# Kernel tuning notes

Hardware: AMD Instinct MI355X
Metric: run time of the kernel (lower is better)

The kernel has to match this reference:

```python
import jax, jax.numpy as jnp
import numpy as np

NUM_POINTS = 2048
FEAT_DIMS = 512
BATCH = 32


def setup_inputs() -> dict:
    key = jax.random.key(0)
    ks = jax.random.split(key, 7)
    glf = jax.random.normal(ks[0], (BATCH, FEAT_DIMS, 1), dtype=jnp.float32)
    # Per-position linear weights (one Conv1d(k=1) per position, fused):
    # W[p, out, in], b[p, out]. Scale like PyTorch Conv1d default init.
    W1 = jax.random.normal(ks[1], (NUM_POINTS, 32, FEAT_DIMS), dtype=jnp.float32) * (1.0 / np.sqrt(FEAT_DIMS))
    b1 = jax.random.normal(ks[2], (NUM_POINTS, 32), dtype=jnp.float32) * 0.01
    W2 = jax.random.normal(ks[3], (NUM_POINTS, 8, 32), dtype=jnp.float32) * (1.0 / np.sqrt(32))
    b2 = jax.random.normal(ks[4], (NUM_POINTS, 8), dtype=jnp.float32) * 0.01
    W3 = jax.random.normal(ks[5], (NUM_POINTS, 3, 8), dtype=jnp.float32) * (1.0 / np.sqrt(8))
    b3 = jax.random.normal(ks[6], (NUM_POINTS, 3), dtype=jnp.float32) * 0.01
    return {"glf": glf, "W1": W1, "b1": b1, "W2": W2, "b2": b2, "W3": W3, "b3": b3}


def _fc_layer(x, W, b):
    # x: [B, Cin, P], W: [P, Cout, Cin], b: [P, Cout] -> [B, Cout, P]
    return jnp.einsum('bip,poi->bop', x, W) + b.T[None, :, :]


def reference(glf, W1, b1, W2, b2, W3, b3):
    # glf: [B, feat_dims, 1] -> repeat along positions
    x = jnp.broadcast_to(glf, (glf.shape[0], glf.shape[1], NUM_POINTS))
    x = _fc_layer(x, W1, b1)  # [B, 32, P]
    x = _fc_layer(x, W2, b2)  # [B, 8, P]
    x = _fc_layer(x, W3, b3)  # [B, 3, P]  (seg_class == 0)
    return x
```

## Files before the change

kernel.cpp:

```cpp
#include <hip/hip_runtime.h>

#define NUM_POINTS 2048
#define FEAT 512
#define BATCH 32
#define POS_PER_BLOCK 2

using v8s = __attribute__((ext_vector_type(8))) short;
using v4f = __attribute__((ext_vector_type(4))) float;

static __device__ __forceinline__ short f2bf(float x) {
  unsigned u = __float_as_uint(x);
  u += 0x7FFFu + ((u >> 16) & 1u);
  return (short)(u >> 16);
}

static __device__ __forceinline__ v8s cvt8(const float* p) {
  float4 f0 = *(const float4*)(p);
  float4 f1 = *(const float4*)(p + 4);
  v8s r;
  r[0] = f2bf(f0.x); r[1] = f2bf(f0.y); r[2] = f2bf(f0.z); r[3] = f2bf(f0.w);
  r[4] = f2bf(f1.x); r[5] = f2bf(f1.y); r[6] = f2bf(f1.z); r[7] = f2bf(f1.w);
  return r;
}

__global__ void build_bfrag(const float* __restrict__ glf, short* __restrict__ frag) {
  int i = blockIdx.x * 256 + threadIdx.x;
  int j = i & 7;
  int l = (i >> 3) & 63;
  int nt = (i >> 9) & 1;
  int ks = i >> 10;
  int b = nt * 16 + (l & 15);
  int k = ks * 32 + ((l >> 4) << 3) + j;
  frag[i] = f2bf(glf[b * FEAT + k]);
}

__global__ void __launch_bounds__(256) fcdec_main(
    const float* __restrict__ W1, const float* __restrict__ b1,
    const float* __restrict__ W2, const float* __restrict__ b2,
    const float* __restrict__ W3, const float* __restrict__ b3,
    const short* __restrict__ bfrag, float* __restrict__ out) {
  __shared__ float h1s[POS_PER_BLOCK][32][33];

  const int t = threadIdx.x;
  const int w = t >> 6;
  const int l = t & 63;
  const int lp = w >> 1;
  const int mt = w & 1;
  const int p = blockIdx.x * POS_PER_BLOCK + lp;
  const int lrow = l & 15;
  const int lk = (l >> 4) << 3;

  v4f acc[2] = {};
  const float* A0 = W1 + ((size_t)p * 32u + mt * 16 + lrow) * FEAT + lk;

  #pragma unroll 4
  for (int ks = 0; ks < 16; ++ks) {
    v8s a = cvt8(A0 + ks * 32);
    v8s bv0 = *(const v8s*)(bfrag + (((ks * 2 + 0) * 64 + l) << 3));
    v8s bv1 = *(const v8s*)(bfrag + (((ks * 2 + 1) * 64 + l) << 3));
    acc[0] = __builtin_amdgcn_mfma_f32_16x16x32_bf16(a, bv0, acc[0], 0, 0, 0);
    acc[1] = __builtin_amdgcn_mfma_f32_16x16x32_bf16(a, bv1, acc[1], 0, 0, 0);
  }

  #pragma unroll
  for (int nt = 0; nt < 2; ++nt)
    #pragma unroll
    for (int r = 0; r < 4; ++r) {
      int o = mt * 16 + ((l >> 4) << 2) + r;
      int b = nt * 16 + (l & 15);
      h1s[lp][o][b] = acc[nt][r] + b1[p * 32 + o];
    }
  __syncthreads();

  if (t < POS_PER_BLOCK * BATCH) {
    const int tp = t >> 5;
    const int b = t & 31;
    const int pg = blockIdx.x * POS_PER_BLOCK + tp;
    float h2[8];
    #pragma unroll
    for (int o8 = 0; o8 < 8; ++o8) {
      float s = b2[pg * 8 + o8];
      const float* w2 = W2 + (size_t)(pg * 8 + o8) * 32;
      #pragma unroll
      for (int i = 0; i < 32; ++i) s += w2[i] * h1s[tp][i][b];
      h2[o8] = s;
    }
    #pragma unroll
    for (int c = 0; c < 3; ++c) {
      float s = b3[pg * 3 + c];
      const float* w3 = W3 + (size_t)(pg * 3 + c) * 8;
      #pragma unroll
      for (int j = 0; j < 8; ++j) s += w3[j] * h2[j];
      out[(size_t)(b * 3 + c) * NUM_POINTS + pg] = s;
    }
  }
}

extern "C" void kernel_launch(void* const* d_in, const int* in_sizes, int n_in,
                              void* d_out, int out_size, void* d_ws, size_t ws_size,
                              hipStream_t stream) {
  const float* glf = (const float*)d_in[0];
  const float* W1  = (const float*)d_in[1];
  const float* b1  = (const float*)d_in[2];
  const float* W2  = (const float*)d_in[3];
  const float* b2  = (const float*)d_in[4];
  const float* W3  = (const float*)d_in[5];
  const float* b3  = (const float*)d_in[6];
  float* out = (float*)d_out;
  short* frag = (short*)d_ws;

  hipLaunchKernelGGL(build_bfrag, dim3(64), dim3(256), 0, stream, glf, frag);
  hipLaunchKernelGGL(fcdec_main, dim3(NUM_POINTS / POS_PER_BLOCK), dim3(256), 0, stream,
                     W1, b1, W2, b2, W3, b3, frag, out);
}
```

Before: 34.31 us.

## Stage W1 tiles into LDS via direct global-to-LDS loads, one position per block

Each block now handles a single position. It bulk-loads that position's 32x512 W1 slice into a 64KB LDS tile using global_load_lds with an XOR swizzle, then each wave reads swizzled float4s from LDS and runs one 16x16 MFMA tile. Layer 2 is spread across all 256 threads, with an extra LDS stage and barrier before layer 3. The aim is wide, coalesced streaming of the dominant W1 traffic. The cost is 64KB of LDS per block, which caps occupancy, plus no overlap between the load phase and the compute phase within a block.

```diff
diff --git a/kernel.cpp b/kernel.cpp
--- a/kernel.cpp
+++ b/kernel.cpp
@@ -3,24 +3,17 @@
 #define NUM_POINTS 2048
 #define FEAT 512
 #define BATCH 32
-#define POS_PER_BLOCK 2
 
 using v8s = __attribute__((ext_vector_type(8))) short;
 using v4f = __attribute__((ext_vector_type(4))) float;
+
+typedef __attribute__((address_space(3))) float lds_f;
+typedef const __attribute__((address_space(1))) float gbl_f;
 
 static __device__ __forceinline__ short f2bf(float x) {
   unsigned u = __float_as_uint(x);
   u += 0x7FFFu + ((u >> 16) & 1u);
   return (short)(u >> 16);
-}
-
-static __device__ __forceinline__ v8s cvt8(const float* p) {
-  float4 f0 = *(const float4*)(p);
-  float4 f1 = *(const float4*)(p + 4);
-  v8s r;
-  r[0] = f2bf(f0.x); r[1] = f2bf(f0.y); r[2] = f2bf(f0.z); r[3] = f2bf(f0.w);
-  r[4] = f2bf(f1.x); r[5] = f2bf(f1.y); r[6] = f2bf(f1.z); r[7] = f2bf(f1.w);
-  return r;
 }
 
 __global__ void build_bfrag(const float* __restrict__ glf, short* __restrict__ frag) {
@@ -34,64 +27,80 @@
   frag[i] = f2bf(glf[b * FEAT + k]);
 }
 
-__global__ void __launch_bounds__(256) fcdec_main(
+__global__ void __launch_bounds__(256, 2) fcdec_main(
     const float* __restrict__ W1, const float* __restrict__ b1,
     const float* __restrict__ W2, const float* __restrict__ b2,
     const float* __restrict__ W3, const float* __restrict__ b3,
     const short* __restrict__ bfrag, float* __restrict__ out) {
-  __shared__ float h1s[POS_PER_BLOCK][32][33];
+  __shared__ float tile[32 * FEAT];
+  __shared__ float h1s[32][33];
+  __shared__ float h2s[8][33];
 
   const int t = threadIdx.x;
   const int w = t >> 6;
   const int l = t & 63;
-  const int lp = w >> 1;
-  const int mt = w & 1;
-  const int p = blockIdx.x * POS_PER_BLOCK + lp;
+  const int p = blockIdx.x;
+  const float* A0 = W1 + (size_t)p * (32u * FEAT);
+
+  #pragma unroll
+  for (int i = 0; i < 16; ++i) {
+    const int rr = i >> 1;
+    const int h = i & 1;
+    const int r = w * 8 + rr;
+    gbl_f* src = (gbl_f*)(A0 + (size_t)r * FEAT + ((h * 64 + (l ^ rr)) << 2));
+    lds_f* dst = (lds_f*)&tile[r * FEAT + h * 256];
+    __builtin_amdgcn_global_load_lds(src, dst, 16, 0, 0);
+  }
+  __syncthreads();
+
+  const int mt = w >> 1;
+  const int nt = w & 1;
   const int lrow = l & 15;
-  const int lk = (l >> 4) << 3;
+  const int g = l >> 4;
+  const int s = l & 7;
+  const int Rbase = (mt * 16 + lrow) * FEAT;
 
-  v4f acc[2] = {};
-  const float* A0 = W1 + ((size_t)p * 32u + mt * 16 + lrow) * FEAT + lk;
-
-  #pragma unroll 4
+  v4f acc = {};
+  #pragma unroll
   for (int ks = 0; ks < 16; ++ks) {
-    v8s a = cvt8(A0 + ks * 32);
-    v8s bv0 = *(const v8s*)(bfrag + (((ks * 2 + 0) * 64 + l) << 3));
-    v8s bv1 = *(const v8s*)(bfrag + (((ks * 2 + 1) * 64 + l) << 3));
-    acc[0] = __builtin_amdgcn_mfma_f32_16x16x32_bf16(a, bv0, acc[0], 0, 0, 0);
-    acc[1] = __builtin_amdgcn_mfma_f32_16x16x32_bf16(a, bv1, acc[1], 0, 0, 0);
+    const int c0 = ks * 8 + g * 2;
+    float4 f0 = *(const float4*)&tile[Rbase + ((c0 ^ s) << 2)];
+    float4 f1 = *(const float4*)&tile[Rbase + (((c0 + 1) ^ s) << 2)];
+    v8s a;
+    a[0] = f2bf(f0.x); a[1] = f2bf(f0.y); a[2] = f2bf(f0.z); a[3] = f2bf(f0.w);
+    a[4] = f2bf(f1.x); a[5] = f2bf(f1.y); a[6] = f2bf(f1.z); a[7] = f2bf(f1.w);
+    v8s bv = *(const v8s*)(bfrag + (((ks * 2 + nt) * 64 + l) << 3));
+    acc = __builtin_amdgcn_mfma_f32_16x16x32_bf16(a, bv, acc, 0, 0, 0);
   }
 
   #pragma unroll
-  for (int nt = 0; nt < 2; ++nt)
-    #pragma unroll
-    for (int r = 0; r < 4; ++r) {
-      int o = mt * 16 + ((l >> 4) << 2) + r;
-      int b = nt * 16 + (l & 15);
-      h1s[lp][o][b] = acc[nt][r] + b1[p * 32 + o];
-    }
+  for (int r4 = 0; r4 < 4; ++r4) {
+    const int o = mt * 16 + g * 4 + r4;
+    const int b = nt * 16 + lrow;
+    h1s[o][b] = acc[r4] + b1[p * 32 + o];
+  }
   __syncthreads();
 
-  if (t < POS_PER_BLOCK * BATCH) {
-    const int tp = t >> 5;
+  {
+    const int o8 = t >> 5;
     const int b = t & 31;
-    const int pg = blockIdx.x * POS_PER_BLOCK + tp;
-    float h2[8];
+    float s2 = b2[p * 8 + o8];
+    const float* w2 = W2 + (size_t)(p * 8 + o8) * 32;
     #pragma unroll
-    for (int o8 = 0; o8 < 8; ++o8) {
-      float s = b2[pg * 8 + o8];
-      const float* w2 = W2 + (size_t)(pg * 8 + o8) * 32;
-      #pragma unroll
-      for (int i = 0; i < 32; ++i) s += w2[i] * h1s[tp][i][b];
-      h2[o8] = s;
-    }
+    for (int i = 0; i < 32; ++i) s2 += w2[i] * h1s[i][b];
+    h2s[o8][b] = s2;
+  }
+  __syncthreads();
+
+  if (t < 32) {
+    const int b = t;
     #pragma unroll
     for (int c = 0; c < 3; ++c) {
-      float s = b3[pg * 3 + c];
-      const float* w3 = W3 + (size_t)(pg * 3 + c) * 8;
+      float s3 = b3[p * 3 + c];
+      const float* w3 = W3 + (size_t)(p * 3 + c) * 8;
       #pragma unroll
-      for (int j = 0; j < 8; ++j) s += w3[j] * h2[j];
-      out[(size_t)(b * 3 + c) * NUM_POINTS + pg] = s;
+      for (int j = 0; j < 8; ++j) s3 += w3[j] * h2s[j][b];
+      out[(size_t)(b * 3 + c) * NUM_POINTS + p] = s3;
     }
   }
 }
@@ -110,6 +119,6 @@
   short* frag = (short*)d_ws;
 
   hipLaunchKernelGGL(build_bfrag, dim3(64), dim3(256), 0, stream, glf, frag);
-  hipLaunchKernelGGL(fcdec_main, dim3(NUM_POINTS / POS_PER_BLOCK), dim3(256), 0, stream,
+  hipLaunchKernelGGL(fcdec_main, dim3(NUM_POINTS), dim3(256), 0, stream,
                      W1, b1, W2, b2, W3, b3, frag, out);
 }
```

Measured after the change: 40.85 us. +19.1%, slower.

## Fuse glf bf16 fragment build into main kernel via shared memory and prefetch W1

Applied to the files above, without the earlier changes.

Drops the separate build_bfrag launch. Each block now converts all of glf (32x512) to bf16 MFMA B-fragments in 32KB of shared memory, and the h1 buffer aliases that memory. All 16 K-steps of W1 loads are issued up front in registers, using two 8-deep halves, so memory latency overlaps the fragment build and the MFMAs. The aim is to remove one launch and the global-memory round trip for the fragments. In exchange every one of the 1024 blocks re-reads 64KB of glf and redoes the conversion. The larger shared memory and register footprint may also limit occupancy.

```diff
diff --git a/kernel.cpp b/kernel.cpp
--- a/kernel.cpp
+++ b/kernel.cpp
@@ -14,32 +14,15 @@
   return (short)(u >> 16);
 }
 
-static __device__ __forceinline__ v8s cvt8(const float* p) {
-  float4 f0 = *(const float4*)(p);
-  float4 f1 = *(const float4*)(p + 4);
-  v8s r;
-  r[0] = f2bf(f0.x); r[1] = f2bf(f0.y); r[2] = f2bf(f0.z); r[3] = f2bf(f0.w);
-  r[4] = f2bf(f1.x); r[5] = f2bf(f1.y); r[6] = f2bf(f1.z); r[7] = f2bf(f1.w);
-  return r;
-}
-
-__global__ void build_bfrag(const float* __restrict__ glf, short* __restrict__ frag) {
-  int i = blockIdx.x * 256 + threadIdx.x;
-  int j = i & 7;
-  int l = (i >> 3) & 63;
-  int nt = (i >> 9) & 1;
-  int ks = i >> 10;
-  int b = nt * 16 + (l & 15);
-  int k = ks * 32 + ((l >> 4) << 3) + j;
-  frag[i] = f2bf(glf[b * FEAT + k]);
-}
-
-__global__ void __launch_bounds__(256) fcdec_main(
+__global__ void __launch_bounds__(256, 4) fcdec_fused(
+    const float* __restrict__ glf,
     const float* __restrict__ W1, const float* __restrict__ b1,
     const float* __restrict__ W2, const float* __restrict__ b2,
     const float* __restrict__ W3, const float* __restrict__ b3,
-    const short* __restrict__ bfrag, float* __restrict__ out) {
-  __shared__ float h1s[POS_PER_BLOCK][32][33];
+    float* __restrict__ out) {
+  __shared__ char smem[32768];
+  short* bfrag = (short*)smem;
+  float (*h1s)[32][33] = (float (*)[32][33])smem;
 
   const int t = threadIdx.x;
   const int w = t >> 6;
@@ -50,26 +33,58 @@
   const int lrow = l & 15;
   const int lk = (l >> 4) << 3;
 
-  v4f acc[2] = {};
   const float* A0 = W1 + ((size_t)p * 32u + mt * 16 + lrow) * FEAT + lk;
 
-  #pragma unroll 4
-  for (int ks = 0; ks < 16; ++ks) {
-    v8s a = cvt8(A0 + ks * 32);
-    v8s bv0 = *(const v8s*)(bfrag + (((ks * 2 + 0) * 64 + l) << 3));
-    v8s bv1 = *(const v8s*)(bfrag + (((ks * 2 + 1) * 64 + l) << 3));
-    acc[0] = __builtin_amdgcn_mfma_f32_16x16x32_bf16(a, bv0, acc[0], 0, 0, 0);
-    acc[1] = __builtin_amdgcn_mfma_f32_16x16x32_bf16(a, bv1, acc[1], 0, 0, 0);
+  float4 fa0[8], fa1[8];
+  #pragma unroll
+  for (int kk = 0; kk < 8; ++kk) {
+    fa0[kk] = *(const float4*)(A0 + kk * 32);
+    fa1[kk] = *(const float4*)(A0 + kk * 32 + 4);
   }
 
   #pragma unroll
-  for (int nt = 0; nt < 2; ++nt)
-    #pragma unroll
-    for (int r = 0; r < 4; ++r) {
-      int o = mt * 16 + ((l >> 4) << 2) + r;
-      int b = nt * 16 + (l & 15);
-      h1s[lp][o][b] = acc[nt][r] + b1[p * 32 + o];
+  for (int rep = 0; rep < 16; ++rep) {
+    int c = rep * 256 + t;
+    int b = c >> 7;
+    int k0 = (c & 127) << 2;
+    float4 g = *(const float4*)(glf + b * FEAT + k0);
+    int ks = k0 >> 5;
+    int gsel = (k0 >> 3) & 3;
+    int j0 = k0 & 7;
+    int nt = b >> 4;
+    int ll = gsel * 16 + (b & 15);
+    short* dst = bfrag + (((ks * 2 + nt) * 64 + ll) << 3) + j0;
+    dst[0] = f2bf(g.x); dst[1] = f2bf(g.y); dst[2] = f2bf(g.z); dst[3] = f2bf(g.w);
+  }
+  __syncthreads();
+
+  v4f acc0 = {}, acc1 = {};
+  #pragma unroll
+  for (int ks = 0; ks < 16; ++ks) {
+    float4 c0 = fa0[ks & 7];
+    float4 c1 = fa1[ks & 7];
+    if (ks < 8) {
+      fa0[ks] = *(const float4*)(A0 + (ks + 8) * 32);
+      fa1[ks] = *(const float4*)(A0 + (ks + 8) * 32 + 4);
     }
+    v8s a;
+    a[0] = f2bf(c0.x); a[1] = f2bf(c0.y); a[2] = f2bf(c0.z); a[3] = f2bf(c0.w);
+    a[4] = f2bf(c1.x); a[5] = f2bf(c1.y); a[6] = f2bf(c1.z); a[7] = f2bf(c1.w);
+    v8s bv0 = *(const v8s*)(bfrag + (((ks * 2 + 0) * 64 + l) << 3));
+    v8s bv1 = *(const v8s*)(bfrag + (((ks * 2 + 1) * 64 + l) << 3));
+    acc0 = __builtin_amdgcn_mfma_f32_16x16x32_bf16(a, bv0, acc0, 0, 0, 0);
+    acc1 = __builtin_amdgcn_mfma_f32_16x16x32_bf16(a, bv1, acc1, 0, 0, 0);
+  }
+
+  __syncthreads();
+
+  #pragma unroll
+  for (int r = 0; r < 4; ++r) {
+    const int o = mt * 16 + ((l >> 4) << 2) + r;
+    const float bb = b1[p * 32 + o];
+    h1s[lp][o][lrow] = acc0[r] + bb;
+    h1s[lp][o][16 + lrow] = acc1[r] + bb;
+  }
   __syncthreads();
 
   if (t < POS_PER_BLOCK * BATCH) {
@@ -107,9 +122,7 @@
   const float* W3  = (const float*)d_in[5];
   const float* b3  = (const float*)d_in[6];
   float* out = (float*)d_out;
-  short* frag = (short*)d_ws;
 
-  hipLaunchKernelGGL(build_bfrag, dim3(64), dim3(256), 0, stream, glf, frag);
-  hipLaunchKernelGGL(fcdec_main, dim3(NUM_POINTS / POS_PER_BLOCK), dim3(256), 0, stream,
-                     W1, b1, W2, b2, W3, b3, frag, out);
+  hipLaunchKernelGGL(fcdec_fused, dim3(NUM_POINTS / POS_PER_BLOCK), dim3(256), 0, stream,
+                     glf, W1, b1, W2, b2, W3, b3, out);
 }
```

New measurement: 31.50 us. 8.2% less time.

## Prefetch W1 halves into registers and LDS via async global_load_lds

Applied to the files above, without the earlier changes.

The first layer now issues every W1 load for a block up front. The first half of the K dimension goes into registers, and the second half is copied asynchronously into an XOR-swizzled LDS buffer with global_load_lds. The bf16 B fragments are also preloaded into registers, so the MFMA loop no longer stalls on each load in turn. The goal is more memory-level parallelism on the bandwidth-bound streaming of W1. In exchange, the block uses much more LDS (64KB, reused for h1s) and more registers, and the LDS reads depend on the compiler inserting the right wait for the async copies.

```diff
diff --git a/kernel.cpp b/kernel.cpp
--- a/kernel.cpp
+++ b/kernel.cpp
@@ -8,19 +8,13 @@
 using v8s = __attribute__((ext_vector_type(8))) short;
 using v4f = __attribute__((ext_vector_type(4))) float;
 
+typedef __attribute__((address_space(3))) float lds_f;
+typedef const __attribute__((address_space(1))) float gbl_f;
+
 static __device__ __forceinline__ short f2bf(float x) {
   unsigned u = __float_as_uint(x);
   u += 0x7FFFu + ((u >> 16) & 1u);
   return (short)(u >> 16);
-}
-
-static __device__ __forceinline__ v8s cvt8(const float* p) {
-  float4 f0 = *(const float4*)(p);
-  float4 f1 = *(const float4*)(p + 4);
-  v8s r;
-  r[0] = f2bf(f0.x); r[1] = f2bf(f0.y); r[2] = f2bf(f0.z); r[3] = f2bf(f0.w);
-  r[4] = f2bf(f1.x); r[5] = f2bf(f1.y); r[6] = f2bf(f1.z); r[7] = f2bf(f1.w);
-  return r;
 }
 
 __global__ void build_bfrag(const float* __restrict__ glf, short* __restrict__ frag) {
@@ -34,12 +28,14 @@
   frag[i] = f2bf(glf[b * FEAT + k]);
 }
 
-__global__ void __launch_bounds__(256) fcdec_main(
+__global__ void __launch_bounds__(256, 2) fcdec_main(
     const float* __restrict__ W1, const float* __restrict__ b1,
     const float* __restrict__ W2, const float* __restrict__ b2,
     const float* __restrict__ W3, const float* __restrict__ b3,
     const short* __restrict__ bfrag, float* __restrict__ out) {
-  __shared__ float h1s[POS_PER_BLOCK][32][33];
+  __shared__ float Ahalf[POS_PER_BLOCK][32][256];
+  float* smem_f = &Ahalf[0][0][0];
+  float (*h1s)[32][33] = (float (*)[32][33])smem_f;
 
   const int t = threadIdx.x;
   const int w = t >> 6;
@@ -48,28 +44,75 @@
   const int mt = w & 1;
   const int p = blockIdx.x * POS_PER_BLOCK + lp;
   const int lrow = l & 15;
-  const int lk = (l >> 4) << 3;
+  const int g = l >> 4;
+  const int lk = g << 3;
+  const int s = lrow & 7;
 
-  v4f acc[2] = {};
   const float* A0 = W1 + ((size_t)p * 32u + mt * 16 + lrow) * FEAT + lk;
+  float4 fa[8], fb[8];
+  #pragma unroll
+  for (int ks = 0; ks < 8; ++ks) {
+    fa[ks] = *(const float4*)(A0 + ks * 32);
+    fb[ks] = *(const float4*)(A0 + ks * 32 + 4);
+  }
 
-  #pragma unroll 4
-  for (int ks = 0; ks < 16; ++ks) {
-    v8s a = cvt8(A0 + ks * 32);
-    v8s bv0 = *(const v8s*)(bfrag + (((ks * 2 + 0) * 64 + l) << 3));
-    v8s bv1 = *(const v8s*)(bfrag + (((ks * 2 + 1) * 64 + l) << 3));
-    acc[0] = __builtin_amdgcn_mfma_f32_16x16x32_bf16(a, bv0, acc[0], 0, 0, 0);
-    acc[1] = __builtin_amdgcn_mfma_f32_16x16x32_bf16(a, bv1, acc[1], 0, 0, 0);
+  v8s bl[8][2];
+  #pragma unroll
+  for (int ks = 0; ks < 8; ++ks) {
+    bl[ks][0] = *(const v8s*)(bfrag + (((ks * 2 + 0) * 64 + l) << 3));
+    bl[ks][1] = *(const v8s*)(bfrag + (((ks * 2 + 1) * 64 + l) << 3));
   }
 
   #pragma unroll
-  for (int nt = 0; nt < 2; ++nt)
-    #pragma unroll
-    for (int r = 0; r < 4; ++r) {
-      int o = mt * 16 + ((l >> 4) << 2) + r;
-      int b = nt * 16 + (l & 15);
-      h1s[lp][o][b] = acc[nt][r] + b1[p * 32 + o];
-    }
+  for (int i = 0; i < 16; ++i) {
+    const int r = mt * 16 + i;
+    gbl_f* src = (gbl_f*)(W1 + ((size_t)p * 32u + r) * FEAT + 256
+                          + ((l ^ (r & 7)) << 2));
+    lds_f* dst = (lds_f*)&Ahalf[lp][r][0];
+    __builtin_amdgcn_global_load_lds(src, dst, 16, 0, 0);
+  }
+
+  v8s bu[8][2];
+  #pragma unroll
+  for (int ks = 0; ks < 8; ++ks) {
+    bu[ks][0] = *(const v8s*)(bfrag + ((((ks + 8) * 2 + 0) * 64 + l) << 3));
+    bu[ks][1] = *(const v8s*)(bfrag + ((((ks + 8) * 2 + 1) * 64 + l) << 3));
+  }
+
+  v4f acc0 = {}, acc1 = {};
+  #pragma unroll
+  for (int ks = 0; ks < 8; ++ks) {
+    v8s a;
+    a[0] = f2bf(fa[ks].x); a[1] = f2bf(fa[ks].y);
+    a[2] = f2bf(fa[ks].z); a[3] = f2bf(fa[ks].w);
+    a[4] = f2bf(fb[ks].x); a[5] = f2bf(fb[ks].y);
+    a[6] = f2bf(fb[ks].z); a[7] = f2bf(fb[ks].w);
+    acc0 = __builtin_amdgcn_mfma_f32_16x16x32_bf16(a, bl[ks][0], acc0, 0, 0, 0);
+    acc1 = __builtin_amdgcn_mfma_f32_16x16x32_bf16(a, bl[ks][1], acc1, 0, 0, 0);
+  }
+
+  const float* Arow = &Ahalf[lp][mt * 16 + lrow][0];
+  #pragma unroll
+  for (int ks = 0; ks < 8; ++ks) {
+    const int c0 = ks * 8 + g * 2;
+    float4 f0 = *(const float4*)(Arow + ((c0 ^ s) << 2));
+    float4 f1 = *(const float4*)(Arow + (((c0 + 1) ^ s) << 2));
+    v8s a;
+    a[0] = f2bf(f0.x); a[1] = f2bf(f0.y); a[2] = f2bf(f0.z); a[3] = f2bf(f0.w);
+    a[4] = f2bf(f1.x); a[5] = f2bf(f1.y); a[6] = f2bf(f1.z); a[7] = f2bf(f1.w);
+    acc0 = __builtin_amdgcn_mfma_f32_16x16x32_bf16(a, bu[ks][0], acc0, 0, 0, 0);
+    acc1 = __builtin_amdgcn_mfma_f32_16x16x32_bf16(a, bu[ks][1], acc1, 0, 0, 0);
+  }
+
+  __syncthreads();
+
+  #pragma unroll
+  for (int r = 0; r < 4; ++r) {
+    const int o = mt * 16 + (g << 2) + r;
+    const float bb = b1[p * 32 + o];
+    h1s[lp][o][lrow] = acc0[r] + bb;
+    h1s[lp][o][16 + lrow] = acc1[r] + bb;
+  }
   __syncthreads();
 
   if (t < POS_PER_BLOCK * BATCH) {
@@ -79,19 +122,19 @@
     float h2[8];
     #pragma unroll
     for (int o8 = 0; o8 < 8; ++o8) {
-      float s = b2[pg * 8 + o8];
+      float sum = b2[pg * 8 + o8];
       const float* w2 = W2 + (size_t)(pg * 8 + o8) * 32;
       #pragma unroll
-      for (int i = 0; i < 32; ++i) s += w2[i] * h1s[tp][i][b];
-      h2[o8] = s;
+      for (int i = 0; i < 32; ++i) sum += w2[i] * h1s[tp][i][b];
+      h2[o8] = sum;
     }
     #pragma unroll
     for (int c = 0; c < 3; ++c) {
-      float s = b3[pg * 3 + c];
+      float sum = b3[pg * 3 + c];
       const float* w3 = W3 + (size_t)(pg * 3 + c) * 8;
       #pragma unroll
-      for (int j = 0; j < 8; ++j) s += w3[j] * h2[j];
-      out[(size_t)(b * 3 + c) * NUM_POINTS + pg] = s;
+      for (int j = 0; j < 8; ++j) sum += w3[j] * h2[j];
+      out[(size_t)(b * 3 + c) * NUM_POINTS + pg] = sum;
     }
   }
 }
```

Measured after the change: 35.03 us. +2.1%, slower.
